# Optimization experiments

Measured on AMD Instinct MI355X. Metric: run time of the kernel, lower is better.

The kernel has to match this reference:

```python
import jax, jax.numpy as jnp
import numpy as np

NUM_HEADS = 8

def setup_inputs() -> dict:
    key = jax.random.key(0)
    ks = jax.random.split(key, 5)
    b, c, h, w = 8, 512, 32, 32
    sd = 1.0 / np.sqrt(c)
    x = jax.random.normal(ks[0], (b, c, h, w), dtype=jnp.float32)
    Wq = jax.random.normal(ks[1], (c, c), dtype=jnp.float32) * sd
    Wk = jax.random.normal(ks[2], (c, c), dtype=jnp.float32) * sd
    Wv = jax.random.normal(ks[3], (c, c), dtype=jnp.float32) * sd
    Wo = jax.random.normal(ks[4], (c, c), dtype=jnp.float32) * sd
    z = jnp.zeros((c,), dtype=jnp.float32)
    return {"x": x, "Wq": Wq, "bq": z, "Wk": Wk, "bk": z, "Wv": Wv, "bv": z, "Wo": Wo, "bo": z}

def reference(x, Wq, bq, Wk, bk, Wv, bv, Wo, bo):
    b, c, h, w = x.shape
    nh = NUM_HEADS
    hd = c // nh
    # [b, c, h, w] -> [b, h*w, c]
    xr = jnp.transpose(x, (0, 2, 3, 1)).reshape(b, h * w, c)
    def proj(W, bias):
        y = xr @ W.T + bias
        return y.reshape(b, h * w, nh, hd)
    q = proj(Wq, bq)  # [b, s, nh, hd]
    k = proj(Wk, bk)
    v = proj(Wv, bv)
    scale = 1.0 / np.sqrt(hd)
    att = jnp.einsum("bsnd,btnd->bnst", q, k) * scale  # [b, nh, s, s]
    att = jax.nn.softmax(att, axis=-1)
    # dropout is identity in eval mode
    out = jnp.einsum("bnst,btnd->bsnd", att, v).reshape(b, h, w, c)
    out = out @ Wo.T + bo  # [b, h, w, c]
    return out
```

## Files before the change

### kernel.cpp

```cpp
#include <hip/hip_runtime.h>

typedef _Float16 half_t;
typedef _Float16 half2v __attribute__((ext_vector_type(2)));
typedef _Float16 half8 __attribute__((ext_vector_type(8)));
typedef float f32x4 __attribute__((ext_vector_type(4)));

static_assert(sizeof(half8) == 16, "half8 must be 16B");

__device__ inline float fast_exp2(float x) {
#if __has_builtin(__builtin_amdgcn_exp2f)
  return __builtin_amdgcn_exp2f(x);
#else
  return exp2f(x);
#endif
}

__device__ inline half2v cvt_pk_f16(float lo, float hi) {
  return __builtin_bit_cast(half2v, __builtin_amdgcn_cvt_pkrtz(lo, hi));
}

__device__ inline void gload_lds16(const void* g, void* l) {
  __builtin_amdgcn_global_load_lds(
      (const __attribute__((address_space(1))) unsigned int*)g,
      (__attribute__((address_space(3))) unsigned int*)l, 16, 0, 0);
}

__global__ void prep_kernel(const float* __restrict__ x,
                            const float* __restrict__ w0, const float* __restrict__ w1,
                            const float* __restrict__ w2, const float* __restrict__ w3,
                            half_t* __restrict__ xr, half_t* __restrict__ wout) {
  if (blockIdx.z < 8) {
    __shared__ float t[32][33];
    const int b = blockIdx.z;
    const int c0 = blockIdx.y * 32;
    const int s0 = blockIdx.x * 32;
    const int tx = threadIdx.x, ty = threadIdx.y;
    const float* xp = x + ((size_t)b * 512 + c0) * 1024 + s0;
#pragma unroll
    for (int r = 0; r < 4; r++) {
      const int cl = ty + 8 * r;
      t[cl][tx] = xp[(size_t)cl * 1024 + tx];
    }
    __syncthreads();
    half_t* op = xr + ((size_t)b * 1024 + s0) * 512 + c0;
#pragma unroll
    for (int r = 0; r < 4; r++) {
      const int sl = ty + 8 * r;
      op[(size_t)sl * 512 + tx] = (half_t)t[tx][sl];
    }
  } else {
    const int f = blockIdx.x + 32 * blockIdx.y;
    const int tid = threadIdx.x + 32 * threadIdx.y;
    const int base = (f * 256 + tid) * 2;
#pragma unroll
    for (int r = 0; r < 2; r++) {
      const int i = base + r;
      const int mz = i >> 16;
      const float* src = (mz == 0) ? w0 : (mz == 1) ? w1 : (mz == 2) ? w2 : w3;
      const float4 v = ((const float4*)src)[i & 65535];
      union { half_t e[4]; unsigned long u; } st;
      st.e[0] = (half_t)v.x; st.e[1] = (half_t)v.y;
      st.e[2] = (half_t)v.z; st.e[3] = (half_t)v.w;
      *(unsigned long*)(wout + (size_t)i * 4) = st.u;
    }
  }
}

template <int MODE, int BM>
__global__ __launch_bounds__(256, 2) void gemm_kernel(
    const half_t* __restrict__ A, const half_t* __restrict__ Wall,
    const float* __restrict__ b0, const float* __restrict__ b1,
    const float* __restrict__ b2, half_t* __restrict__ qkv,
    float* __restrict__ fout) {
  constexpr int K = 512;
  constexpr int IREP = BM / 32;
  __shared__ alignas(16) half_t lA[BM * 64];
  __shared__ alignas(16) half_t lB[128 * 64];

  int bx, by, bz;
  {
    const int flat = blockIdx.x + gridDim.x * (blockIdx.y + gridDim.y * blockIdx.z);
    const int xcd = flat & 7;
    const int r = flat >> 3;
    if (MODE == 0) {
      bx = r & 3; bz = (r >> 2) % 3; by = (r / 12) * 8 + xcd;
    } else {
      bx = r & 3; bz = 0; by = (r >> 2) * 8 + xcd;
    }
  }

  const int z = bz;
  const half_t* W = Wall + (size_t)z * K * 512;
  const float* bias = (MODE == 1) ? b0 : (z == 0 ? b0 : (z == 1 ? b1 : b2));

  const int tid = threadIdx.x;
  const int lane = tid & 63;
  const int wid = tid >> 6;
  const int wm = wid >> 1, wn = wid & 1;
  const int g = lane >> 4, r16 = lane & 15;
  const int m0 = by * BM, n0 = bx * 128;

  f32x4 acc[IREP][4];
#pragma unroll
  for (int i = 0; i < IREP; i++)
#pragma unroll
    for (int j = 0; j < 4; j++) acc[i][j] = (f32x4){0.f, 0.f, 0.f, 0.f};

  for (int k0 = 0; k0 < K; k0 += 64) {
#pragma unroll
    for (int t = 0; t < BM / 32; t++) {
      const int o = (t * 256 + tid) * 16;
      const int row = o >> 7;
      const int kbs = (o & 127) ^ ((row & 7) << 4);
      gload_lds16((const char*)(A + (size_t)(m0 + row) * K + k0) + kbs, (char*)lA + o);
    }
#pragma unroll
    for (int t = 0; t < 4; t++) {
      const int o = (t * 256 + tid) * 16;
      const int row = o >> 7;
      const int kbs = (o & 127) ^ ((row & 7) << 4);
      gload_lds16((const char*)(W + (size_t)(n0 + row) * K + k0) + kbs, (char*)lB + o);
    }
    __syncthreads();
#pragma unroll
    for (int kk = 0; kk < 2; kk++) {
      half8 af[IREP], bf[4];
#pragma unroll
      for (int i = 0; i < IREP; i++) {
        const int row = wm * (BM / 2) + i * 16 + r16;
        const int sw = (row & 7) << 4;
        af[i] = *(const half8*)((const char*)lA + row * 128 + ((kk * 64 + g * 16) ^ sw));
      }
#pragma unroll
      for (int j = 0; j < 4; j++) {
        const int row = wn * 64 + j * 16 + r16;
        const int sw = (row & 7) << 4;
        bf[j] = *(const half8*)((const char*)lB + row * 128 + ((kk * 64 + g * 16) ^ sw));
      }
#pragma unroll
      for (int i = 0; i < IREP; i++)
#pragma unroll
        for (int j = 0; j < 4; j++)
          acc[i][j] = __builtin_amdgcn_mfma_f32_16x16x32_f16(af[i], bf[j], acc[i][j], 0, 0, 0);
    }
    __syncthreads();
  }

  half_t* dst = (MODE == 0) ? (qkv + (size_t)z * 4194304) : (half_t*)nullptr;
  const float scale = (MODE == 0 && z == 0) ? 0.18033688011112042f : 1.0f;
#pragma unroll
  for (int i = 0; i < IREP; i++) {
#pragma unroll
    for (int j = 0; j < 4; j++) {
      const int n = n0 + wn * 64 + j * 16 + r16;
      const float bvv = bias[n];
      const int mb = m0 + wm * (BM / 2) + i * 16 + g * 4;
      if (MODE == 0 && z == 2) {
        const int bb = mb >> 10, s0v = mb & 1023, hh = n >> 6, d = n & 63;
        const int kvb = s0v & 31;
        const int sp0 = (s0v & ~31) | ((((kvb & 15) >> 2) << 3) + ((kvb >> 4) << 2));
        half_t* dp = dst + (size_t)(bb * 8 + hh) * 65536 + ((size_t)d << 10) + sp0;
        union { half_t e[4]; unsigned long u; } st;
#pragma unroll
        for (int rr = 0; rr < 4; rr++) st.e[rr] = (half_t)(acc[i][j][rr] + bvv);
        *(unsigned long*)dp = st.u;
      } else {
#pragma unroll
        for (int rr = 0; rr < 4; rr++) {
          const int m = mb + rr;
          const float v = (acc[i][j][rr] + bvv) * scale;
          if (MODE == 0) {
            const int bb = m >> 10, s = m & 1023, hh = n >> 6, d = n & 63;
            dst[(((size_t)(bb * 8 + hh) * 1024 + s) << 6) + d] = (half_t)v;
          } else {
            fout[(size_t)m * 512 + n] = v;
          }
        }
      }
    }
  }
}


__device__ inline half8 lds_frag128(const half_t* l, int row, int cb) {
  const char* p = (const char*)l + row * 128 + (cb ^ ((row & 7) << 4));
  return *(const half8*)p;
}

__device__ inline half8 lds_frag256(const half_t* l, int row, int cb) {
  const char* p = (const char*)l + row * 256 + (cb ^ ((row & 7) << 4));
  return *(const half8*)p;
}

__global__ __launch_bounds__(256) void attn_kernel(
    const half_t* __restrict__ Q, const half_t* __restrict__ Kh,
    const half_t* __restrict__ V, half_t* __restrict__ O) {
  __shared__ alignas(16) half_t lK[2][128 * 64];
  __shared__ alignas(16) half_t lV[2][64 * 128];

  const int tid = threadIdx.x;
  const int lane = tid & 63;
  const int w = tid >> 6;
  const int flat = blockIdx.x + (blockIdx.y << 3);
  const int xcd = flat & 7;
  const int tt = flat >> 3;
  const int qch = tt & 7;
  const int bh = ((tt >> 3) << 3) | xcd;
  const int b = bh >> 3, h = bh & 7;
  const int g = lane >> 4, r16 = lane & 15;
  const size_t base = (size_t)bh * 65536;
  const half_t* Qp = Q + base;
  const half_t* Kp = Kh + base;
  const half_t* Vt = V + base;
  const int q0 = qch * 128 + w * 32;

  half8 qf[2][2];
#pragma unroll
  for (int qt = 0; qt < 2; qt++) {
    const half_t* qrow = Qp + (size_t)(q0 + qt * 16 + r16) * 64 + g * 8;
    qf[qt][0] = *(const half8*)(qrow);
    qf[qt][1] = *(const half8*)(qrow + 32);
  }

  f32x4 acc[2][4];
#pragma unroll
  for (int qt = 0; qt < 2; qt++)
#pragma unroll
    for (int i = 0; i < 4; i++) acc[qt][i] = (f32x4){0.f, 0.f, 0.f, 0.f};
  float lsum[2] = {0.f, 0.f};

  auto stage = [&](int kv0, int bufi) {
    half_t* lk = lK[bufi];
    half_t* lv = lV[bufi];
    const char* ksrc = (const char*)(Kp + (size_t)kv0 * 64);
    const char* vsrc = (const char*)Vt + (size_t)kv0 * 2;
#pragma unroll
    for (int i = 0; i < 4; i++) {
      const int o = i * 4096 + tid * 16;
      const int krow = o >> 7;
      const int kcs = (o & 127) ^ ((krow & 7) << 4);
      gload_lds16(ksrc + krow * 128 + kcs, (char*)lk + o);
      const int vrow = o >> 8;
      const int vcs = (o & 255) ^ ((vrow & 7) << 4);
      gload_lds16(vsrc + vrow * 2048 + vcs, (char*)lv + o);
    }
  };

  stage(0, 0);
  __syncthreads();

  int buf = 0;
  for (int kv0 = 0; kv0 < 1024; kv0 += 128) {
    if (kv0 + 128 < 1024) stage(kv0 + 128, buf ^ 1);
    const half_t* lk = lK[buf];
    const half_t* lv = lV[buf];
#pragma unroll
    for (int sub = 0; sub < 4; sub++) {
      half8 kf0 = lds_frag128(lk, sub * 32 + r16, g * 16);
      half8 kf1 = lds_frag128(lk, sub * 32 + r16, 64 + g * 16);
      half8 kf2 = lds_frag128(lk, sub * 32 + 16 + r16, g * 16);
      half8 kf3 = lds_frag128(lk, sub * 32 + 16 + r16, 64 + g * 16);
      half8 vf[4];
#pragma unroll
      for (int dt = 0; dt < 4; dt++)
        vf[dt] = lds_frag256(lv, dt * 16 + r16, sub * 64 + g * 16);

      f32x4 s[2][2];
      __builtin_amdgcn_s_setprio(1);
#pragma unroll
      for (int qt = 0; qt < 2; qt++) {
        s[qt][0] = (f32x4){0.f, 0.f, 0.f, 0.f};
        s[qt][1] = (f32x4){0.f, 0.f, 0.f, 0.f};
        s[qt][0] = __builtin_amdgcn_mfma_f32_16x16x32_f16(kf0, qf[qt][0], s[qt][0], 0, 0, 0);
        s[qt][0] = __builtin_amdgcn_mfma_f32_16x16x32_f16(kf1, qf[qt][1], s[qt][0], 0, 0, 0);
        s[qt][1] = __builtin_amdgcn_mfma_f32_16x16x32_f16(kf2, qf[qt][0], s[qt][1], 0, 0, 0);
        s[qt][1] = __builtin_amdgcn_mfma_f32_16x16x32_f16(kf3, qf[qt][1], s[qt][1], 0, 0, 0);
      }
      __builtin_amdgcn_s_setprio(0);

      union { half8 v; half2v h2[4]; } pu[2];
#pragma unroll
      for (int qt = 0; qt < 2; qt++) {
        float p[8];
#pragma unroll
        for (int i = 0; i < 4; i++) {
          p[i] = fast_exp2(s[qt][0][i]);
          p[4 + i] = fast_exp2(s[qt][1][i]);
        }
        lsum[qt] += ((p[0] + p[1]) + (p[2] + p[3])) + ((p[4] + p[5]) + (p[6] + p[7]));
#pragma unroll
        for (int i = 0; i < 4; i++)
          pu[qt].h2[i] = cvt_pk_f16(p[2 * i], p[2 * i + 1]);
      }

      __builtin_amdgcn_s_setprio(1);
#pragma unroll
      for (int qt = 0; qt < 2; qt++)
#pragma unroll
        for (int dt = 0; dt < 4; dt++)
          acc[qt][dt] = __builtin_amdgcn_mfma_f32_16x16x32_f16(vf[dt], pu[qt].v, acc[qt][dt], 0, 0, 0);
      __builtin_amdgcn_s_setprio(0);
    }
    __syncthreads();
    buf ^= 1;
  }

#pragma unroll
  for (int qt = 0; qt < 2; qt++) {
    float l = lsum[qt];
    l += __shfl_xor(l, 16);
    l += __shfl_xor(l, 32);
    const float inv = 1.f / l;
    half_t* orow = O + ((size_t)b * 1024 + q0 + qt * 16 + r16) * 512 + h * 64;
#pragma unroll
    for (int dt = 0; dt < 4; dt++) {
      union { half_t e[4]; unsigned long u; } st;
#pragma unroll
      for (int rr = 0; rr < 4; rr++) st.e[rr] = (half_t)(acc[qt][dt][rr] * inv);
      *(unsigned long*)(orow + dt * 16 + g * 4) = st.u;
    }
  }
}

extern "C" void kernel_launch(void* const* d_in, const int* in_sizes, int n_in,
                              void* d_out, int out_size, void* d_ws, size_t ws_size,
                              hipStream_t stream) {
  if (ws_size < 44040192u) return;
  const float* x  = (const float*)d_in[0];
  const float* Wq = (const float*)d_in[1];
  const float* bq = (const float*)d_in[2];
  const float* Wk = (const float*)d_in[3];
  const float* bk = (const float*)d_in[4];
  const float* Wv = (const float*)d_in[5];
  const float* bv = (const float*)d_in[6];
  const float* Wo = (const float*)d_in[7];
  const float* bo = (const float*)d_in[8];
  char* ws = (char*)d_ws;
  half_t* xr = (half_t*)(ws + 0);
  half_t* W4 = (half_t*)(ws + 8388608);
  half_t* Qb = (half_t*)(ws + 10485760);
  half_t* AO = (half_t*)(ws + 35651584);
  float* out = (float*)d_out;

  prep_kernel<<<dim3(32, 16, 9), dim3(32, 8), 0, stream>>>(x, Wq, Wk, Wv, Wo, xr, W4);
  gemm_kernel<0, 128><<<dim3(4, 64, 3), 256, 0, stream>>>(xr, W4, bq, bk, bv, Qb, nullptr);
  attn_kernel<<<dim3(8, 64), 256, 0, stream>>>(Qb, Qb + 4194304, Qb + 8388608, AO);
  gemm_kernel<1, 64><<<dim3(4, 128, 1), 256, 0, stream>>>(AO, W4 + 786432, bo, nullptr, nullptr,
                                                          nullptr, out);
}
```

Measured before the change: 68.03 us.

## Double-buffer GEMM LDS tiles and vectorize epilogue via swapped MFMA operands

Adds a second LDS buffer to the projection GEMM so the next K-tile is loaded with global_load_lds while the current tile feeds MFMAs, keeping one barrier per iteration. For Q/K and the output projection it swaps the MFMA A/B operands so each lane holds four consecutive output columns, which allows vectorized bias loads and 8-byte or 16-byte stores instead of scalar strided stores. The cost is doubled LDS per block, which may lower occupancy against the launch bound of two blocks per CU.

```diff
diff --git a/kernel.cpp b/kernel.cpp
--- a/kernel.cpp
+++ b/kernel.cpp
@@ -74,8 +74,8 @@
     float* __restrict__ fout) {
   constexpr int K = 512;
   constexpr int IREP = BM / 32;
-  __shared__ alignas(16) half_t lA[BM * 64];
-  __shared__ alignas(16) half_t lB[128 * 64];
+  __shared__ alignas(16) half_t lA[2][BM * 64];
+  __shared__ alignas(16) half_t lB[2][128 * 64];
 
   int bx, by, bz;
   {
@@ -106,22 +106,29 @@
 #pragma unroll
     for (int j = 0; j < 4; j++) acc[i][j] = (f32x4){0.f, 0.f, 0.f, 0.f};
 
-  for (int k0 = 0; k0 < K; k0 += 64) {
+  auto stage = [&](int k0, int bi) {
 #pragma unroll
     for (int t = 0; t < BM / 32; t++) {
       const int o = (t * 256 + tid) * 16;
       const int row = o >> 7;
       const int kbs = (o & 127) ^ ((row & 7) << 4);
-      gload_lds16((const char*)(A + (size_t)(m0 + row) * K + k0) + kbs, (char*)lA + o);
+      gload_lds16((const char*)(A + (size_t)(m0 + row) * K + k0) + kbs, (char*)lA[bi] + o);
     }
 #pragma unroll
     for (int t = 0; t < 4; t++) {
       const int o = (t * 256 + tid) * 16;
       const int row = o >> 7;
       const int kbs = (o & 127) ^ ((row & 7) << 4);
-      gload_lds16((const char*)(W + (size_t)(n0 + row) * K + k0) + kbs, (char*)lB + o);
-    }
-    __syncthreads();
+      gload_lds16((const char*)(W + (size_t)(n0 + row) * K + k0) + kbs, (char*)lB[bi] + o);
+    }
+  };
+
+  stage(0, 0);
+  __syncthreads();
+
+  int buf = 0;
+  for (int k0 = 0; k0 < K; k0 += 64) {
+    if (k0 + 64 < K) stage(k0 + 64, buf ^ 1);
 #pragma unroll
     for (int kk = 0; kk < 2; kk++) {
       half8 af[IREP], bf[4];
@@ -129,21 +136,30 @@
       for (int i = 0; i < IREP; i++) {
         const int row = wm * (BM / 2) + i * 16 + r16;
         const int sw = (row & 7) << 4;
-        af[i] = *(const half8*)((const char*)lA + row * 128 + ((kk * 64 + g * 16) ^ sw));
+        af[i] = *(const half8*)((const char*)lA[buf] + row * 128 + ((kk * 64 + g * 16) ^ sw));
       }
 #pragma unroll
       for (int j = 0; j < 4; j++) {
         const int row = wn * 64 + j * 16 + r16;
         const int sw = (row & 7) << 4;
-        bf[j] = *(const half8*)((const char*)lB + row * 128 + ((kk * 64 + g * 16) ^ sw));
-      }
-#pragma unroll
-      for (int i = 0; i < IREP; i++)
-#pragma unroll
-        for (int j = 0; j < 4; j++)
-          acc[i][j] = __builtin_amdgcn_mfma_f32_16x16x32_f16(af[i], bf[j], acc[i][j], 0, 0, 0);
+        bf[j] = *(const half8*)((const char*)lB[buf] + row * 128 + ((kk * 64 + g * 16) ^ sw));
+      }
+      if (MODE == 0 && z == 2) {
+#pragma unroll
+        for (int i = 0; i < IREP; i++)
+#pragma unroll
+          for (int j = 0; j < 4; j++)
+            acc[i][j] = __builtin_amdgcn_mfma_f32_16x16x32_f16(af[i], bf[j], acc[i][j], 0, 0, 0);
+      } else {
+#pragma unroll
+        for (int i = 0; i < IREP; i++)
+#pragma unroll
+          for (int j = 0; j < 4; j++)
+            acc[i][j] = __builtin_amdgcn_mfma_f32_16x16x32_f16(bf[j], af[i], acc[i][j], 0, 0, 0);
+      }
     }
     __syncthreads();
+    buf ^= 1;
   }
 
   half_t* dst = (MODE == 0) ? (qkv + (size_t)z * 4194304) : (half_t*)nullptr;
@@ -152,10 +168,10 @@
   for (int i = 0; i < IREP; i++) {
 #pragma unroll
     for (int j = 0; j < 4; j++) {
-      const int n = n0 + wn * 64 + j * 16 + r16;
-      const float bvv = bias[n];
-      const int mb = m0 + wm * (BM / 2) + i * 16 + g * 4;
       if (MODE == 0 && z == 2) {
+        const int n = n0 + wn * 64 + j * 16 + r16;
+        const float bvv = bias[n];
+        const int mb = m0 + wm * (BM / 2) + i * 16 + g * 4;
         const int bb = mb >> 10, s0v = mb & 1023, hh = n >> 6, d = n & 63;
         const int kvb = s0v & 31;
         const int sp0 = (s0v & ~31) | ((((kvb & 15) >> 2) << 3) + ((kvb >> 4) << 2));
@@ -165,16 +181,22 @@
         for (int rr = 0; rr < 4; rr++) st.e[rr] = (half_t)(acc[i][j][rr] + bvv);
         *(unsigned long*)dp = st.u;
       } else {
-#pragma unroll
-        for (int rr = 0; rr < 4; rr++) {
-          const int m = mb + rr;
-          const float v = (acc[i][j][rr] + bvv) * scale;
-          if (MODE == 0) {
-            const int bb = m >> 10, s = m & 1023, hh = n >> 6, d = n & 63;
-            dst[(((size_t)(bb * 8 + hh) * 1024 + s) << 6) + d] = (half_t)v;
-          } else {
-            fout[(size_t)m * 512 + n] = v;
-          }
+        const int n4 = n0 + wn * 64 + j * 16 + g * 4;
+        const float4 b4 = *(const float4*)(bias + n4);
+        const int m = m0 + wm * (BM / 2) + i * 16 + r16;
+        if (MODE == 0) {
+          const int bb = m >> 10, s = m & 1023, hh = n4 >> 6, d = n4 & 63;
+          union { half_t e[4]; unsigned long u; } st;
+          st.e[0] = (half_t)((acc[i][j][0] + b4.x) * scale);
+          st.e[1] = (half_t)((acc[i][j][1] + b4.y) * scale);
+          st.e[2] = (half_t)((acc[i][j][2] + b4.z) * scale);
+          st.e[3] = (half_t)((acc[i][j][3] + b4.w) * scale);
+          *(unsigned long*)(dst + (((size_t)(bb * 8 + hh) * 1024 + s) << 6) + d) = st.u;
+        } else {
+          float4 v;
+          v.x = acc[i][j][0] + b4.x; v.y = acc[i][j][1] + b4.y;
+          v.z = acc[i][j][2] + b4.z; v.w = acc[i][j][3] + b4.w;
+          *(float4*)(fout + (size_t)m * 512 + n4) = v;
         }
       }
     }
```

Result: slower. 86.43 us (+27.1%).

## Double-buffer GEMM LDS tiles with async global-to-LDS prefetch two stages ahead

Applied to the files above, without the earlier changes.

Converts the projection GEMM's K loop from a single LDS buffer with load-sync-compute-sync into a two-buffer pipeline. The next tile is loaded through global_load_lds while MFMAs run on the current one, with explicit vmcnt waits and barriers. This is meant to hide global memory latency behind compute. LDS use doubles, which may cut occupancy under launch_bounds(256,2), and the hand-written vmcnt counts must match the number of loads issued.

```diff
diff --git a/kernel.cpp b/kernel.cpp
--- a/kernel.cpp
+++ b/kernel.cpp
@@ -74,8 +74,9 @@
     float* __restrict__ fout) {
   constexpr int K = 512;
   constexpr int IREP = BM / 32;
-  __shared__ alignas(16) half_t lA[BM * 64];
-  __shared__ alignas(16) half_t lB[128 * 64];
+  constexpr int NT = K / 64;
+  __shared__ alignas(16) half_t lA[2][BM * 64];
+  __shared__ alignas(16) half_t lB[2][128 * 64];
 
   int bx, by, bz;
   {
@@ -106,44 +107,71 @@
 #pragma unroll
     for (int j = 0; j < 4; j++) acc[i][j] = (f32x4){0.f, 0.f, 0.f, 0.f};
 
-  for (int k0 = 0; k0 < K; k0 += 64) {
+  auto stage = [&](int k0, int bi) {
 #pragma unroll
     for (int t = 0; t < BM / 32; t++) {
       const int o = (t * 256 + tid) * 16;
       const int row = o >> 7;
       const int kbs = (o & 127) ^ ((row & 7) << 4);
-      gload_lds16((const char*)(A + (size_t)(m0 + row) * K + k0) + kbs, (char*)lA + o);
+      gload_lds16((const char*)(A + (size_t)(m0 + row) * K + k0) + kbs, (char*)lA[bi] + o);
     }
 #pragma unroll
     for (int t = 0; t < 4; t++) {
       const int o = (t * 256 + tid) * 16;
       const int row = o >> 7;
       const int kbs = (o & 127) ^ ((row & 7) << 4);
-      gload_lds16((const char*)(W + (size_t)(n0 + row) * K + k0) + kbs, (char*)lB + o);
-    }
-    __syncthreads();
+      gload_lds16((const char*)(W + (size_t)(n0 + row) * K + k0) + kbs, (char*)lB[bi] + o);
+    }
+  };
+
+  stage(0, 0);
+  stage(64, 1);
+  if constexpr (BM == 128) asm volatile("s_waitcnt vmcnt(8)" ::: "memory");
+  else                     asm volatile("s_waitcnt vmcnt(6)" ::: "memory");
+  __builtin_amdgcn_sched_barrier(0);
+  __builtin_amdgcn_s_barrier();
+
+  int buf = 0;
+#pragma unroll 1
+  for (int t = 0; t < NT; ++t) {
+    half8 af[2][IREP], bf[2][4];
 #pragma unroll
     for (int kk = 0; kk < 2; kk++) {
-      half8 af[IREP], bf[4];
 #pragma unroll
       for (int i = 0; i < IREP; i++) {
         const int row = wm * (BM / 2) + i * 16 + r16;
         const int sw = (row & 7) << 4;
-        af[i] = *(const half8*)((const char*)lA + row * 128 + ((kk * 64 + g * 16) ^ sw));
+        af[kk][i] = *(const half8*)((const char*)lA[buf] + row * 128 + ((kk * 64 + g * 16) ^ sw));
       }
 #pragma unroll
       for (int j = 0; j < 4; j++) {
         const int row = wn * 64 + j * 16 + r16;
         const int sw = (row & 7) << 4;
-        bf[j] = *(const half8*)((const char*)lB + row * 128 + ((kk * 64 + g * 16) ^ sw));
-      }
+        bf[kk][j] = *(const half8*)((const char*)lB[buf] + row * 128 + ((kk * 64 + g * 16) ^ sw));
+      }
+    }
+    asm volatile("s_waitcnt lgkmcnt(0)" ::: "memory");
+    __builtin_amdgcn_sched_barrier(0);
+    __builtin_amdgcn_s_barrier();
+    if (t + 2 < NT) stage((t + 2) * 64, buf);
+#pragma unroll
+    for (int kk = 0; kk < 2; kk++)
 #pragma unroll
       for (int i = 0; i < IREP; i++)
 #pragma unroll
         for (int j = 0; j < 4; j++)
-          acc[i][j] = __builtin_amdgcn_mfma_f32_16x16x32_f16(af[i], bf[j], acc[i][j], 0, 0, 0);
-    }
-    __syncthreads();
+          acc[i][j] = __builtin_amdgcn_mfma_f32_16x16x32_f16(af[kk][i], bf[kk][j], acc[i][j], 0, 0, 0);
+    if (t + 2 < NT) {
+      if constexpr (BM == 128) asm volatile("s_waitcnt vmcnt(8)" ::: "memory");
+      else                     asm volatile("s_waitcnt vmcnt(6)" ::: "memory");
+      __builtin_amdgcn_sched_barrier(0);
+      __builtin_amdgcn_s_barrier();
+    } else if (t + 1 < NT) {
+      asm volatile("s_waitcnt vmcnt(0)" ::: "memory");
+      __builtin_amdgcn_sched_barrier(0);
+      __builtin_amdgcn_s_barrier();
+    }
+    buf ^= 1;
   }
 
   half_t* dst = (MODE == 0) ? (qkv + (size_t)z * 4194304) : (half_t*)nullptr;
```

After: 68.94 us. Within noise of the previous version (+1.3%).
